# Kernel optimization log

Measured on AMD Instinct MI355X. Metric: run time of the kernel, lower is better.

## Reference

```python
import jax, jax.numpy as jnp
import numpy as np

NHEAD = 8
TOPKS = (8, 8)  # topk per level, coarse -> fine


def _to_bshd(x):
    # [B, C, H, W] -> [B, H*W, nhead, d]  (matches rearrange 'b c h w -> b (h w) c' + view)
    b, c, h, w = x.shape
    return jnp.transpose(x.reshape(b, c, h * w), (0, 2, 1)).reshape(b, h * w, NHEAD, c // NHEAD)


def _coarse_level(q, k, v, topk):
    b, c, h, w = k.shape
    d = c // NHEAD
    q_, k_, v_ = _to_bshd(q), _to_bshd(k), _to_bshd(v)
    temp = 1.0 / (d ** 0.5)
    A = jax.nn.softmax(jnp.einsum('nlhd,nshd->nlsh', q_, k_) * temp, axis=2)  # [b,L,S,h]
    _, idx = jax.lax.top_k(jnp.swapaxes(A, 2, 3), topk)  # [b,L,h,k]
    idx = jnp.swapaxes(idx, 2, 3)                        # [b,L,k,h]
    msg = jnp.einsum('nlsh,nshd->nlhd', A, v_)           # [b,L,h,d]
    topk_pos = jnp.stack([idx // w, idx % w])            # [2,b,L,k,h]
    return msg, topk_pos


def _fine_level(q, k, v, topk_pos, topk_prev, topk):
    b, c, h0, w0 = q.shape
    w1 = k.shape[3]
    d = c // NHEAD
    k_, v_ = _to_bshd(k), _to_bshd(v)
    H2, W2 = h0 // 2, w0 // 2
    L0 = H2 * W2
    # query grouped into 2x2 quads: [b, L0, 4, h, d]
    q_ = q.reshape(b, c, H2, 2, W2, 2).transpose(0, 2, 4, 3, 5, 1).reshape(b, L0, 4, NHEAD, d)
    tp = topk_pos * 2  # coarse positions -> fine grid
    cand = [(tp[0] + x) * w1 + tp[1] + y for x in (0, 1) for y in (0, 1)]
    t2 = topk_prev * 4
    idx = jnp.stack(cand, axis=3).reshape(b, L0, t2, NHEAD)  # [b,L,t2,h]
    idx_bh = idx.transpose(0, 3, 1, 2).reshape(b, NHEAD, L0 * t2)

    def gather(p):  # p: [b,S,h,d] -> gathered [b,L,t2,h,d]
        g = jnp.take_along_axis(jnp.swapaxes(p, 1, 2), idx_bh[..., None], axis=2)
        return g.reshape(b, NHEAD, L0, t2, d).transpose(0, 2, 3, 1, 4)

    tk, tv = gather(k_), gather(v_)
    temp = 1.0 / (d ** 0.5)
    A = jax.nn.softmax(jnp.einsum('blqhd,blthd->blqth', q_, tk) * temp, axis=3)  # [b,L,4,t2,h]
    _, ti = jax.lax.top_k(jnp.moveaxis(A, 3, 4), topk)  # [b,L,4,h,k]
    ti = jnp.moveaxis(ti, 4, 3)                         # [b,L,4,k,h]
    msg = jnp.einsum('blqth,blthd->blqhd', A, tv)       # [b,L,4,h,d]
    idx_b = jnp.broadcast_to(idx[:, :, None], (b, L0, 4, t2, NHEAD))
    gidx = jnp.take_along_axis(idx_b, ti, axis=3)       # [b,L,4,k,h] flat fine-grid indices
    gidx = gidx.reshape(b, H2, W2, 2, 2, topk, NHEAD).transpose(0, 1, 3, 2, 4, 5, 6)
    gidx = gidx.reshape(b, h0 * w0, topk, NHEAD)
    return msg, gidx


def _forward(q_fine, q_coarse, k_fine, k_coarse, v_fine, v_coarse, weight):
    msg0, topk_pos = _coarse_level(q_coarse, k_coarse, v_coarse, TOPKS[0])
    msg1, _ = _fine_level(q_fine, k_fine, v_fine, topk_pos, TOPKS[0], TOPKS[1])
    w = jax.nn.softmax(weight, axis=0)
    fm = msg0 * w[0]                  # [b,Lc,h,d]
    fm = fm[:, :, None] + msg1 * w[1]  # [b,Lc,4,h,d]
    b, Hc, Wc = q_coarse.shape[0], q_coarse.shape[2], q_coarse.shape[3]
    d = fm.shape[-1]
    # rearrange 'b (H W) (t1 t2) h d -> b (H t1 W t2) h d'
    fm = fm.reshape(b, Hc, Wc, 2, 2, NHEAD, d).transpose(0, 1, 3, 2, 4, 5, 6)
    return fm.reshape(b, Hc * Wc * 4, NHEAD, d)


def setup_inputs() -> dict:
    key = jax.random.key(0)
    ks = jax.random.split(key, 7)
    B, C = 4, 128
    return {
        'q_fine': jax.random.normal(ks[0], (B, C, 64, 64), jnp.float32),
        'q_coarse': jax.random.normal(ks[1], (B, C, 32, 32), jnp.float32),
        'k_fine': jax.random.normal(ks[2], (B, C, 64, 64), jnp.float32),
        'k_coarse': jax.random.normal(ks[3], (B, C, 32, 32), jnp.float32),
        'v_fine': jax.random.normal(ks[4], (B, C, 64, 64), jnp.float32),
        'v_coarse': jax.random.normal(ks[5], (B, C, 32, 32), jnp.float32),
        'weight': jax.random.normal(ks[6], (2,), jnp.float32),
    }


def reference(q_fine, q_coarse, k_fine, k_coarse, v_fine, v_coarse, weight):
    return _forward(q_fine, q_coarse, k_fine, k_coarse, v_fine, v_coarse, weight)
```

## Files before the change

kernel.cpp:

```cpp
#include <hip/hip_runtime.h>
#include <stdint.h>

#define TEMP 0.25f

typedef unsigned short u16;
typedef short v8s __attribute__((ext_vector_type(8)));
typedef float v4f __attribute__((ext_vector_type(4)));

static __device__ __forceinline__ uint32_t f2b_bits(float f){
    union { float f; uint32_t i; } x; x.f = f;
    uint32_t u = x.i;
    return (u + 0x7FFFu + ((u >> 16) & 1u)) >> 16;
}
static __device__ __forceinline__ float b2f(u16 u){
    union { uint32_t i; float f; } x; x.i = ((uint32_t)u) << 16; return x.f;
}
static __device__ __forceinline__ float bl(uint32_t u){
    union { uint32_t i; float f; } x; x.i = u << 16; return x.f;
}
static __device__ __forceinline__ float bh(uint32_t u){
    union { uint32_t i; float f; } x; x.i = u & 0xffff0000u; return x.f;
}
static __device__ __forceinline__ uint4 pack8(const uint32_t* e){
    return make_uint4(e[0] | (e[1] << 16), e[2] | (e[3] << 16),
                      e[4] | (e[5] << 16), e[6] | (e[7] << 16));
}
union U8S { uint4 u; v8s s; };
union I4S { int i[4]; v8s s; };
static __device__ __forceinline__ v8s asv8s(uint4 u){ U8S x; x.u = u; return x.s; }

template<int C>
static __device__ __forceinline__ float dppf(float x){
    int xi = __float_as_int(x);
    return __int_as_float(__builtin_amdgcn_update_dpp(xi, xi, C, 0xf, 0xf, false));
}
static __device__ __forceinline__ float red16_max(float m){
    m = fmaxf(m, dppf<0xB1>(m));  m = fmaxf(m, dppf<0x4E>(m));
    m = fmaxf(m, dppf<0x141>(m)); m = fmaxf(m, dppf<0x140>(m));
    return m;
}
static __device__ __forceinline__ float red16_sum(float s){
    s += dppf<0xB1>(s);  s += dppf<0x4E>(s);
    s += dppf<0x141>(s); s += dppf<0x140>(s);
    return s;
}
template<int C>
static __device__ __forceinline__ uint64_t dppmax64(uint64_t k){
    int hi = (int)(uint32_t)(k >> 32), lo = (int)(uint32_t)k;
    uint32_t oh = (uint32_t)__builtin_amdgcn_update_dpp(hi, hi, C, 0xf, 0xf, false);
    uint32_t ol = (uint32_t)__builtin_amdgcn_update_dpp(lo, lo, C, 0xf, 0xf, false);
    uint64_t ok = ((uint64_t)oh << 32) | ol;
    return ok > k ? ok : k;
}
static __device__ __forceinline__ uint64_t red16_maxkey(uint64_t k){
    k = dppmax64<0xB1>(k);  k = dppmax64<0x4E>(k);
    k = dppmax64<0x141>(k); k = dppmax64<0x140>(k);
    return k;
}

__global__ __launch_bounds__(256)
void pack_coarse(const float* __restrict__ kc, const float* __restrict__ vc,
                 uint4* __restrict__ KP1, uint4* __restrict__ KP3,
                 uint4* __restrict__ VP1)
{
    const int bh = blockIdx.x;
    const int kv = blockIdx.y;
    const int z  = blockIdx.z;
    const int b = bh >> 3, h = bh & 7;
    const int tid = threadIdx.x;
    const size_t sbase = (size_t)(b * 128 + h * 16) * 1024;
    const size_t fbase = (size_t)bh * 64 * 64;

    #pragma unroll
    for (int it = 0; it < 2; ++it){
        int task = it * 256 + tid;
        int kt = z * 8 + (task >> 6), ln = task & 63;
        int quad = ln >> 4, col = ln & 15;
        if (kv == 0){
            uint32_t e1[8], e3[8];
            #pragma unroll
            for (int j = 0; j < 8; ++j){
                int dch = (quad & 1) * 8 + j;
                float x = kc[sbase + (size_t)dch * 1024 + kt * 16 + col];
                uint32_t u0 = f2b_bits(x);
                float r1 = x - b2f((u16)u0);
                uint32_t u1 = f2b_bits(r1);
                float r2 = r1 - b2f((u16)u1);
                uint32_t u2 = f2b_bits(r2);
                e1[j] = (quad < 2) ? u0 : u1;
                e3[j] = (quad < 2) ? u2 : u0;
            }
            KP1[fbase + kt * 64 + ln] = pack8(e1);
            KP3[fbase + kt * 64 + ln] = pack8(e3);
        } else {
            uint32_t e[8];
            #pragma unroll
            for (int j = 0; j < 8; ++j){
                int key = kt * 16 + (quad & 1) * 8 + j;
                float x = vc[sbase + (size_t)col * 1024 + key];
                uint32_t u0 = f2b_bits(x);
                uint32_t u1 = f2b_bits(x - b2f((u16)u0));
                e[j] = (quad < 2) ? u0 : u1;
            }
            VP1[fbase + kt * 64 + ln] = pack8(e);
        }
    }
}

__global__ __launch_bounds__(256)
void pack_all(const float* __restrict__ kf, const float* __restrict__ vf,
              const float* __restrict__ qf,
              const float* __restrict__ kc, const float* __restrict__ vc,
              uint32_t* __restrict__ packed, float* __restrict__ qT,
              uint4* __restrict__ KP1, uint4* __restrict__ KP3,
              uint4* __restrict__ VP1)
{
    __shared__ float tile[64][129];
    const int bid = blockIdx.x;
    const int tid = threadIdx.x;

    if (bid < 768){
        const int pt = bid & 63, b = (bid >> 6) & 3, z = bid >> 8;
        const float* src = (z == 0) ? kf : (z == 1) ? vf : qf;
        const int pos0 = pt * 64;

        #pragma unroll
        for (int it = 0; it < 8; ++it){
            int task = it * 256 + tid;
            int ch = task >> 4, p4 = task & 15;
            float4 v = *(const float4*)(src + (size_t)(b * 128 + ch) * 4096 + pos0 + p4 * 4);
            tile[p4*4+0][ch] = v.x; tile[p4*4+1][ch] = v.y;
            tile[p4*4+2][ch] = v.z; tile[p4*4+3][ch] = v.w;
        }
        __syncthreads();

        if (z == 2){
            #pragma unroll
            for (int it = 0; it < 8; ++it){
                int task = it * 256 + tid;
                int p = task >> 5, c4 = task & 31;
                float4 v = make_float4(tile[p][c4*4+0], tile[p][c4*4+1],
                                       tile[p][c4*4+2], tile[p][c4*4+3]);
                *(float4*)(qT + ((size_t)(b * 4096) + pos0 + p) * 128 + c4 * 4) = v;
            }
        } else {
            const int x = pt;
            #pragma unroll
            for (int it = 0; it < 2; ++it){
                int task = it * 256 + tid;
                int hq = task >> 6, y = task & 63;
                int pprime = ((x >> 1) * 32 + (y >> 1)) * 4 + (x & 1) * 2 + (y & 1);
                size_t line = (size_t)(b * 8 + hq) * 4096 + pprime;
                uint32_t dw[8];
                #pragma unroll
                for (int i = 0; i < 8; ++i){
                    uint32_t lo = f2b_bits(tile[y][hq * 16 + 2 * i]);
                    uint32_t hi = f2b_bits(tile[y][hq * 16 + 2 * i + 1]);
                    dw[i] = lo | (hi << 16);
                }
                uint4* dst4 = (uint4*)packed + line * 4 + z * 2;
                dst4[0] = make_uint4(dw[0], dw[1], dw[2], dw[3]);
                dst4[1] = make_uint4(dw[4], dw[5], dw[6], dw[7]);
            }
        }
    } else {
        const int f2 = bid - 768;
        const int bh = f2 & 31, kv = (f2 >> 5) & 1, z = f2 >> 6;
        const int b = bh >> 3, h = bh & 7;
        const size_t sbase = (size_t)(b * 128 + h * 16) * 1024;
        const size_t fbase = (size_t)bh * 64 * 64;

        #pragma unroll
        for (int it = 0; it < 2; ++it){
            int task = it * 256 + tid;
            int kt = z * 8 + (task >> 6), ln = task & 63;
            int quad = ln >> 4, col = ln & 15;
            if (kv == 0){
                uint32_t e1[8], e3[8];
                #pragma unroll
                for (int j = 0; j < 8; ++j){
                    int dch = (quad & 1) * 8 + j;
                    float x = kc[sbase + (size_t)dch * 1024 + kt * 16 + col];
                    uint32_t u0 = f2b_bits(x);
                    float r1 = x - b2f((u16)u0);
                    uint32_t u1 = f2b_bits(r1);
                    float r2 = r1 - b2f((u16)u1);
                    uint32_t u2 = f2b_bits(r2);
                    e1[j] = (quad < 2) ? u0 : u1;
                    e3[j] = (quad < 2) ? u2 : u0;
                }
                KP1[fbase + kt * 64 + ln] = pack8(e1);
                KP3[fbase + kt * 64 + ln] = pack8(e3);
            } else {
                uint32_t e[8];
                #pragma unroll
                for (int j = 0; j < 8; ++j){
                    int key = kt * 16 + (quad & 1) * 8 + j;
                    float x = vc[sbase + (size_t)col * 1024 + key];
                    uint32_t xb = __float_as_uint(x);
                    uint32_t u0 = xb >> 16;
                    uint32_t u1 = f2b_bits(x - b2f((u16)u0));
                    e[j] = (quad < 2) ? u0 : u1;
                }
                VP1[fbase + kt * 64 + ln] = pack8(e);
            }
        }
    }
}

__global__ __launch_bounds__(256)
void coarse_mfma(const float* __restrict__ qc,
                 const uint4* __restrict__ KP1, const uint4* __restrict__ KP3,
                 const uint4* __restrict__ VP1,
                 float* __restrict__ msg0, int* __restrict__ topk_out)
{
    const int ltile = blockIdx.x;
    const int h = blockIdx.y, b = blockIdx.z;
    const int bh = b * 8 + h;
    const int tid = threadIdx.x, lane = tid & 63, wv = tid >> 6;
    const int quad = lane >> 4, col = lane & 15;
    const int lanex = lane ^ 32;
    const int lbase = ltile * 16;

    __shared__ uint32_t tls[4][16 * 20];
    __shared__ float rred[2][4][16];
    __shared__ float pvred[4][16][16];
    __shared__ float tkv[4][16][8];
    __shared__ int   tki[4][16][8];

    v8s a1, a3;
    {
        int row = lbase + col;
        int dch0 = (quad & 1) * 8;
        #pragma unroll
        for (int j = 0; j < 8; ++j){
            float x = qc[(size_t)(b * 128 + h * 16 + dch0 + j) * 1024 + row] * TEMP;
            uint32_t u0 = f2b_bits(x);
            float r1 = x - b2f((u16)u0);
            uint32_t u1 = f2b_bits(r1);
            float r2 = r1 - b2f((u16)u1);
            uint32_t u2 = f2b_bits(r2);
            a1[j] = (short)(quad < 2 ? u0 : u1);
            a3[j] = (short)(quad < 2 ? u0 : u2);
        }
    }

    const size_t fbase = (size_t)bh * 64 * 64;
    v4f sc[16];
    #pragma unroll
    for (int kt = 0; kt < 16; ++kt){
        int ktg = wv * 16 + kt;
        v8s b1 = asv8s(KP1[fbase + (size_t)ktg * 64 + lane]);
        v8s b2 = asv8s(KP1[fbase + (size_t)ktg * 64 + lanex]);
        v8s b3 = asv8s(KP3[fbase + (size_t)ktg * 64 + lane]);
        v4f c = {0.f, 0.f, 0.f, 0.f};
        c = __builtin_amdgcn_mfma_f32_16x16x32_bf16(a1, b1, c, 0, 0, 0);
        c = __builtin_amdgcn_mfma_f32_16x16x32_bf16(a1, b2, c, 0, 0, 0);
        c = __builtin_amdgcn_mfma_f32_16x16x32_bf16(a3, b3, c, 0, 0, 0);
        sc[kt] = c;
    }

    #pragma unroll
    for (int r = 0; r < 4; ++r){
        float m = sc[0][r];
        #pragma unroll
        for (int kt = 1; kt < 16; ++kt) m = fmaxf(m, sc[kt][r]);
        m = red16_max(m);
        if (col == 0) rred[0][wv][quad * 4 + r] = m;
    }
    __syncthreads();
    #pragma unroll
    for (int r = 0; r < 4; ++r){
        int row = quad * 4 + r;
        float m = fmaxf(fmaxf(rred[0][0][row], rred[0][1][row]),
                        fmaxf(rred[0][2][row], rred[0][3][row]));
        #pragma unroll
        for (int kt = 0; kt < 16; ++kt) sc[kt][r] = __expf(sc[kt][r] - m);
    }
    #pragma unroll
    for (int r = 0; r < 4; ++r){
        float s = 0.f;
        #pragma unroll
        for (int kt = 0; kt < 16; ++kt) s += sc[kt][r];
        s = red16_sum(s);
        if (col == 0) rred[1][wv][quad * 4 + r] = s;
    }

    v4f acc = {0.f, 0.f, 0.f, 0.f};
    uint32_t* tw = tls[wv];
    const int rdbase = col * 20 + 8 * (quad & 1);
    const uint32_t selp = (quad < 2) ? 0x05040100u : 0x07060302u;
    #pragma unroll
    for (int kt = 0; kt < 16; ++kt){
        #pragma unroll
        for (int r = 0; r < 4; ++r){
            float x = sc[kt][r];
            uint32_t u0 = __float_as_uint(x) >> 16;
            uint32_t u1 = f2b_bits(x - b2f((u16)u0));
            tw[(quad * 4 + r) * 20 + col] = u0 | (u1 << 16);
        }
        __builtin_amdgcn_s_waitcnt(0xC07F);
        uint4 d0 = *(const uint4*)&tw[rdbase];
        uint4 d1 = *(const uint4*)&tw[rdbase + 4];
        I4S ux;
        ux.i[0] = __builtin_amdgcn_perm(d0.y, d0.x, selp);
        ux.i[1] = __builtin_amdgcn_perm(d0.w, d0.z, selp);
        ux.i[2] = __builtin_amdgcn_perm(d1.y, d1.x, selp);
        ux.i[3] = __builtin_amdgcn_perm(d1.w, d1.z, selp);
        v8s ap = ux.s;
        v8s bv1 = asv8s(VP1[fbase + (size_t)(wv * 16 + kt) * 64 + lane]);
        v8s bv2 = asv8s(VP1[fbase + (size_t)(wv * 16 + kt) * 64 + lanex]);
        acc = __builtin_amdgcn_mfma_f32_16x16x32_bf16(ap, bv1, acc, 0, 0, 0);
        acc = __builtin_amdgcn_mfma_f32_16x16x32_bf16(ap, bv2, acc, 0, 0, 0);
    }
    #pragma unroll
    for (int r = 0; r < 4; ++r) pvred[wv][quad * 4 + r][col] = acc[r];

    #pragma unroll
    for (int r = 0; r < 4; ++r){
        int row = quad * 4 + r;
        #pragma unroll
        for (int rnd = 0; rnd < 8; ++rnd){
            float bv = sc[0][r]; int bk = 0;
            #pragma unroll
            for (int kt = 1; kt < 16; ++kt){
                bool g = sc[kt][r] > bv;
                bv = g ? sc[kt][r] : bv; bk = g ? kt : bk;
            }
            int bi = bk * 16 + col;
            uint64_t k = ((uint64_t)(uint32_t)__float_as_int(bv) << 32)
                       | (uint32_t)(~bi);
            k = red16_maxkey(k);
            bv = __int_as_float((int)(uint32_t)(k >> 32));
            bi = (int)(~(uint32_t)k);
            if ((bi & 15) == col){
                int ktw = bi >> 4;
                #pragma unroll
                for (int kt = 0; kt < 16; ++kt)
                    if (kt == ktw) sc[kt][r] = -1.0f;
            }
            if (col == rnd){ tkv[wv][row][rnd] = bv; tki[wv][row][rnd] = wv * 256 + bi; }
        }
    }
    __syncthreads();

    {
        int row = tid >> 4, dd = tid & 15;
        float v = pvred[0][row][dd] + pvred[1][row][dd] +
                  pvred[2][row][dd] + pvred[3][row][dd];
        float s = rred[1][0][row] + rred[1][1][row] +
                  rred[1][2][row] + rred[1][3][row];
        msg0[((size_t)((b * 1024 + lbase + row) * 8 + h)) * 16 + dd] = v / s;
    }
    if (tid < 16){
        int row = tid;
        int* tp = topk_out + (((b * 1024 + lbase + row) * 8 + h) * 8);
        int p[4] = {0, 0, 0, 0};
        #pragma unroll
        for (int rnd = 0; rnd < 8; ++rnd){
            float bv = -3.0f; int bw = 0, bi = 0x7fffffff;
            #pragma unroll
            for (int w = 0; w < 4; ++w){
                float v = tkv[w][row][p[w]];
                int   i = tki[w][row][p[w]];
                bool g = (v > bv) || (v == bv && i < bi);
                bv = g ? v : bv; bi = g ? i : bi; bw = g ? w : bw;
            }
            tp[rnd] = bi;
            p[bw]++;
        }
    }
}

__global__ __launch_bounds__(512, 2)
void coarse_kernel(const float* __restrict__ qc, const float* __restrict__ kc,
                   const float* __restrict__ vc, float* __restrict__ msg0,
                   int* __restrict__ topk_out)
{
    const int ltile = blockIdx.x;
    const int h = blockIdx.y, b = blockIdx.z;
    const int tid = threadIdx.x;
    const int lane = tid & 63, wv = tid >> 6;
    const int lbase = ltile * 32;
    __shared__ float sKV[16 * 1024];
    const size_t base = (size_t)(b * 128 + h * 16) * 1024;
    {
        const float4* gK = (const float4*)(kc + base);
        float4* lK = (float4*)sKV;
        #pragma unroll
        for (int i = 0; i < 8; ++i) lK[tid + 512 * i] = gK[tid + 512 * i];
    }
    float qreg[4];
    {
        int dq = lane & 15;
        #pragma unroll
        for (int li = 0; li < 4; ++li){
            int l = lbase + wv * 4 + li;
            qreg[li] = qc[base + (size_t)dq * 1024 + l] * TEMP;
        }
    }
    __syncthreads();
    float p[4][16];
    #pragma unroll
    for (int li = 0; li < 4; ++li)
        #pragma unroll
        for (int j = 0; j < 16; ++j) p[li][j] = 0.f;
    #pragma unroll
    for (int dch = 0; dch < 16; ++dch){
        float kf[16];
        #pragma unroll
        for (int ch = 0; ch < 4; ++ch){
            float4 kv = *(const float4*)&sKV[dch * 1024 + ch * 256 + (lane << 2)];
            kf[ch*4+0] = kv.x; kf[ch*4+1] = kv.y; kf[ch*4+2] = kv.z; kf[ch*4+3] = kv.w;
        }
        float qs[4];
        #pragma unroll
        for (int li = 0; li < 4; ++li) qs[li] = __shfl(qreg[li], dch);
        #pragma unroll
        for (int li = 0; li < 4; ++li)
            #pragma unroll
            for (int j = 0; j < 16; ++j) p[li][j] = fmaf(qs[li], kf[j], p[li][j]);
    }
    float invs[4];
    #pragma unroll
    for (int li = 0; li < 4; ++li){
        float m = p[li][0];
        #pragma unroll
        for (int j = 1; j < 16; ++j) m = fmaxf(m, p[li][j]);
        #pragma unroll
        for (int off = 32; off > 0; off >>= 1) m = fmaxf(m, __shfl_xor(m, off));
        float s = 0.f;
        #pragma unroll
        for (int j = 0; j < 16; ++j){ p[li][j] = __expf(p[li][j] - m); s += p[li][j]; }
        #pragma unroll
        for (int off = 32; off > 0; off >>= 1) s += __shfl_xor(s, off);
        invs[li] = 1.0f / s;
    }
    __syncthreads();
    {
        const float4* gV = (const float4*)(vc + base);
        float4* lV = (float4*)sKV;
        #pragma unroll
        for (int i = 0; i < 8; ++i) lV[tid + 512 * i] = gV[tid + 512 * i];
    }
    __syncthreads();
    float outv = 0.f;
    #pragma unroll
    for (int dd = 0; dd < 16; ++dd){
        float vf[16];
        #pragma unroll
        for (int ch = 0; ch < 4; ++ch){
            float4 vv = *(const float4*)&sKV[dd * 1024 + ch * 256 + (lane << 2)];
            vf[ch*4+0] = vv.x; vf[ch*4+1] = vv.y; vf[ch*4+2] = vv.z; vf[ch*4+3] = vv.w;
        }
        float a[4];
        #pragma unroll
        for (int li = 0; li < 4; ++li){
            float s = 0.f;
            #pragma unroll
            for (int j = 0; j < 16; ++j) s = fmaf(p[li][j], vf[j], s);
            a[li] = s;
        }
        #pragma unroll
        for (int off = 32; off > 0; off >>= 1)
            #pragma unroll
            for (int li = 0; li < 4; ++li) a[li] += __shfl_xor(a[li], off);
        #pragma unroll
        for (int li = 0; li < 4; ++li)
            outv = (lane == li * 16 + dd) ? a[li] * invs[li] : outv;
    }
    {
        int li = lane >> 4, dd = lane & 15;
        int l = lbase + wv * 4 + li;
        msg0[(size_t)((b * 1024 + l) * 8 + h) * 16 + dd] = outv;
    }
    const int lanebase = lane << 4;
    int mytk = 0;
    for (int r = 0; r < 8; ++r){
        float bv[4]; int bi[4];
        #pragma unroll
        for (int li = 0; li < 4; ++li){
            float v0[8]; int j0[8];
            #pragma unroll
            for (int k = 0; k < 8; ++k){
                bool g = p[li][2*k+1] > p[li][2*k];
                v0[k] = g ? p[li][2*k+1] : p[li][2*k];
                j0[k] = g ? 2*k+1 : 2*k;
            }
            float v1[4]; int j1[4];
            #pragma unroll
            for (int k = 0; k < 4; ++k){
                bool g = v0[2*k+1] > v0[2*k];
                v1[k] = g ? v0[2*k+1] : v0[2*k];
                j1[k] = g ? j0[2*k+1] : j0[2*k];
            }
            float v2[2]; int j2[2];
            #pragma unroll
            for (int k = 0; k < 2; ++k){
                bool g = v1[2*k+1] > v1[2*k];
                v2[k] = g ? v1[2*k+1] : v1[2*k];
                j2[k] = g ? j1[2*k+1] : j1[2*k];
            }
            bool g3 = v2[1] > v2[0];
            bv[li] = g3 ? v2[1] : v2[0];
            bi[li] = lanebase | (g3 ? j2[1] : j2[0]);
        }
        #pragma unroll
        for (int off = 32; off > 0; off >>= 1){
            #pragma unroll
            for (int li = 0; li < 4; ++li){
                float ov = __shfl_xor(bv[li], off);
                int   oi = __shfl_xor(bi[li], off);
                bool g = (ov > bv[li]) || (ov == bv[li] && oi < bi[li]);
                bv[li] = g ? ov : bv[li];
                bi[li] = g ? oi : bi[li];
            }
        }
        #pragma unroll
        for (int li = 0; li < 4; ++li){
            #pragma unroll
            for (int j = 0; j < 16; ++j)
                p[li][j] = (bi[li] == (lanebase | j)) ? -1.0f : p[li][j];
            mytk = (lane == li * 8 + r) ? bi[li] : mytk;
        }
    }
    if (lane < 32){
        int li = lane >> 3, r = lane & 7;
        int jw = mytk & 15, lw = mytk >> 4;
        int s = ((jw >> 2) << 8) | (lw << 2) | (jw & 3);
        int l = lbase + wv * 4 + li;
        topk_out[((b * 1024 + l) * 8 + h) * 8 + r] = s;
    }
}

__global__ __launch_bounds__(256)
void pack_kernel(const float* __restrict__ kf, const float* __restrict__ vf,
                 const float* __restrict__ qf,
                 uint32_t* __restrict__ packed, float* __restrict__ qT)
{
    const int pt = blockIdx.x;
    const int b  = blockIdx.y;
    const int z  = blockIdx.z;
    const float* src = (z == 0) ? kf : (z == 1) ? vf : qf;
    const int tid = threadIdx.x;
    __shared__ float tile[64][129];
    const int pos0 = pt * 64;

    #pragma unroll
    for (int it = 0; it < 8; ++it){
        int task = it * 256 + tid;
        int ch = task >> 4, p4 = task & 15;
        float4 v = *(const float4*)(src + (size_t)(b * 128 + ch) * 4096 + pos0 + p4 * 4);
        tile[p4*4+0][ch] = v.x; tile[p4*4+1][ch] = v.y;
        tile[p4*4+2][ch] = v.z; tile[p4*4+3][ch] = v.w;
    }
    __syncthreads();

    if (z == 2){
        #pragma unroll
        for (int it = 0; it < 8; ++it){
            int task = it * 256 + tid;
            int p = task >> 5, c4 = task & 31;
            float4 v = make_float4(tile[p][c4*4+0], tile[p][c4*4+1],
                                   tile[p][c4*4+2], tile[p][c4*4+3]);
            *(float4*)(qT + ((size_t)(b * 4096) + pos0 + p) * 128 + c4 * 4) = v;
        }
    } else {
        const int x = pt;
        #pragma unroll
        for (int it = 0; it < 2; ++it){
            int task = it * 256 + tid;
            int h = task >> 6, y = task & 63;
            int pprime = ((x >> 1) * 32 + (y >> 1)) * 4 + (x & 1) * 2 + (y & 1);
            size_t line = (size_t)(b * 8 + h) * 4096 + pprime;
            uint32_t dw[8];
            #pragma unroll
            for (int i = 0; i < 8; ++i){
                uint32_t lo = f2b_bits(tile[y][h * 16 + 2 * i]);
                uint32_t hi = f2b_bits(tile[y][h * 16 + 2 * i + 1]);
                dw[i] = lo | (hi << 16);
            }
            uint4* dst4 = (uint4*)packed + line * 4 + z * 2;
            dst4[0] = make_uint4(dw[0], dw[1], dw[2], dw[3]);
            dst4[1] = make_uint4(dw[4], dw[5], dw[6], dw[7]);
        }
    }
}

__global__ __launch_bounds__(256)
void fine_kernel(const float* __restrict__ qf, const float* __restrict__ kf,
                 const float* __restrict__ vf,
                 const float* __restrict__ qTg, const uint32_t* __restrict__ packed,
                 int transposed,
                 const float* __restrict__ wt,
                 const int* __restrict__ topk_in, const float* __restrict__ msg0,
                 float* __restrict__ out)
{
    const int l0 = blockIdx.x;
    const int b  = blockIdx.y;
    const int tid = threadIdx.x;

    __shared__ float vT[8][16][34];
    __shared__ float qT[8][4][16];
    __shared__ float pT[8][4][32];
    __shared__ int tkS[8][8];

    if (tid < 64) tkS[tid >> 3][tid & 7] =
        topk_in[((b * 1024 + l0) * 8 + (tid >> 3)) * 8 + (tid & 7)];
    __syncthreads();

    const int i = l0 >> 5, j = l0 & 31;
    const int hh = tid >> 5;
    const int t  = tid & 31;
    const int kk = t >> 2, cp = t & 3;

    float k[16];
    {
        int s = tkS[hh][kk];
        if (transposed){
            const uint4* pk = (const uint4*)packed;
            size_t line = (size_t)(b * 8 + hh) * 4096 + s * 4 + cp;
            uint4 a0 = pk[line*4+0], a1 = pk[line*4+1];
            uint4 a2 = pk[line*4+2], a3 = pk[line*4+3];
            k[0]=bl(a0.x);  k[1]=bh(a0.x);  k[2]=bl(a0.y);  k[3]=bh(a0.y);
            k[4]=bl(a0.z);  k[5]=bh(a0.z);  k[6]=bl(a0.w);  k[7]=bh(a0.w);
            k[8]=bl(a1.x);  k[9]=bh(a1.x);  k[10]=bl(a1.y); k[11]=bh(a1.y);
            k[12]=bl(a1.z); k[13]=bh(a1.z); k[14]=bl(a1.w); k[15]=bh(a1.w);
            vT[hh][0][t]=bl(a2.x);  vT[hh][1][t]=bh(a2.x);
            vT[hh][2][t]=bl(a2.y);  vT[hh][3][t]=bh(a2.y);
            vT[hh][4][t]=bl(a2.z);  vT[hh][5][t]=bh(a2.z);
            vT[hh][6][t]=bl(a2.w);  vT[hh][7][t]=bh(a2.w);
            vT[hh][8][t]=bl(a3.x);  vT[hh][9][t]=bh(a3.x);
            vT[hh][10][t]=bl(a3.y); vT[hh][11][t]=bh(a3.y);
            vT[hh][12][t]=bl(a3.z); vT[hh][13][t]=bh(a3.z);
            vT[hh][14][t]=bl(a3.w); vT[hh][15][t]=bh(a3.w);
        } else {
            int pos = (2 * (s >> 5) + (cp >> 1)) * 64 + 2 * (s & 31) + (cp & 1);
            size_t gb = (size_t)(b * 128 + hh * 16) * 4096 + pos;
            #pragma unroll
            for (int ch = 0; ch < 16; ++ch){
                k[ch] = kf[gb + (size_t)ch * 4096];
                vT[hh][ch][t] = vf[gb + (size_t)ch * 4096];
            }
        }
    }
    if (tid < 128){
        int qh = tid >> 4, aq = (tid >> 2) & 3, c4 = tid & 3;
        int qpos = (2 * i + (aq >> 1)) * 64 + 2 * j + (aq & 1);
        if (transposed){
            float4 u = *(const float4*)(qTg + ((size_t)(b * 4096) + qpos) * 128 + qh * 16 + c4 * 4);
            qT[qh][aq][c4*4+0] = u.x * TEMP;
            qT[qh][aq][c4*4+1] = u.y * TEMP;
            qT[qh][aq][c4*4+2] = u.z * TEMP;
            qT[qh][aq][c4*4+3] = u.w * TEMP;
        } else {
            #pragma unroll
            for (int c = 0; c < 4; ++c)
                qT[qh][aq][c4*4+c] =
                    qf[(size_t)(b * 128 + qh * 16 + c4 * 4 + c) * 4096 + qpos] * TEMP;
        }
    }
    __syncthreads();

    {
        float sc[4] = {0.f, 0.f, 0.f, 0.f};
        #pragma unroll
        for (int dch = 0; dch < 16; ++dch){
            float kv = k[dch];
            #pragma unroll
            for (int q = 0; q < 4; ++q) sc[q] = fmaf(qT[hh][q][dch], kv, sc[q]);
        }
        #pragma unroll
        for (int q = 0; q < 4; ++q){
            float m = sc[q];
            #pragma unroll
            for (int off = 16; off > 0; off >>= 1) m = fmaxf(m, __shfl_xor(m, off, 32));
            float e = __expf(sc[q] - m);
            float s = e;
            #pragma unroll
            for (int off = 16; off > 0; off >>= 1) s += __shfl_xor(s, off, 32);
            pT[hh][q][t] = e / s;
        }
    }
    __syncthreads();

    {
        float w0 = wt[0], w1 = wt[1];
        float mx = fmaxf(w0, w1);
        float e0 = __expf(w0 - mx), e1 = __expf(w1 - mx);
        float w0f = e0 / (e0 + e1), w1f = e1 / (e0 + e1);

        int q0 = (tid >> 4) & 1;
        int dd = tid & 15;
        float a0 = 0.f, a1 = 0.f;
        #pragma unroll
        for (int tt = 0; tt < 16; ++tt){
            float v0 = vT[hh][dd][tt * 2], v1 = vT[hh][dd][tt * 2 + 1];
            float2 pA = *(const float2*)&pT[hh][q0][tt * 2];
            float2 pB = *(const float2*)&pT[hh][q0 + 2][tt * 2];
            a0 = fmaf(pA.x, v0, a0); a0 = fmaf(pA.y, v1, a0);
            a1 = fmaf(pB.x, v0, a1); a1 = fmaf(pB.y, v1, a1);
        }
        float m0 = msg0[(size_t)((b * 1024 + l0) * 8 + hh) * 16 + dd];
        float o0 = w0f * m0 + w1f * a0;
        float o1 = w0f * m0 + w1f * a1;
        int posA = (2 * i) * 64 + 2 * j + q0;
        int posB = (2 * i + 1) * 64 + 2 * j + q0;
        out[(size_t)((b * 4096 + posA) * 8 + hh) * 16 + dd] = o0;
        out[(size_t)((b * 4096 + posB) * 8 + hh) * 16 + dd] = o1;
    }
}

extern "C" void kernel_launch(void* const* d_in, const int* in_sizes, int n_in,
                              void* d_out, int out_size, void* d_ws, size_t ws_size,
                              hipStream_t stream)
{
    (void)in_sizes; (void)n_in; (void)out_size;

    const float* q_fine   = (const float*)d_in[0];
    const float* q_coarse = (const float*)d_in[1];
    const float* k_fine   = (const float*)d_in[2];
    const float* k_coarse = (const float*)d_in[3];
    const float* v_fine   = (const float*)d_in[4];
    const float* v_coarse = (const float*)d_in[5];
    const float* weight   = (const float*)d_in[6];

    const size_t MB = 1024 * 1024;
    float*    msg0   = (float*)d_ws;
    int*      topk   = (int*)((char*)d_ws + 2 * MB);
    float*    qT     = (float*)((char*)d_ws + 3 * MB);
    uint32_t* packed = (uint32_t*)((char*)d_ws + 11 * MB);
    uint4*    KP1    = (uint4*)((char*)d_ws + 19 * MB);
    uint4*    KP3    = (uint4*)((char*)d_ws + 21 * MB);
    uint4*    VP1    = (uint4*)((char*)d_ws + 23 * MB);
    const int doT = (ws_size >= 19 * MB) ? 1 : 0;
    const int doM = (ws_size >= 25 * MB) ? 1 : 0;

    if (doM && doT){
        pack_all<<<dim3(1280), dim3(256), 0, stream>>>(k_fine, v_fine, q_fine,
                                                       k_coarse, v_coarse,
                                                       packed, qT, KP1, KP3, VP1);
        coarse_mfma<<<dim3(64, 8, 4), dim3(256), 0, stream>>>(q_coarse, KP1, KP3, VP1,
                                                              msg0, topk);
    } else {
        if (doM){
            pack_coarse<<<dim3(32, 2, 8), dim3(256), 0, stream>>>(k_coarse, v_coarse,
                                                                  KP1, KP3, VP1);
            coarse_mfma<<<dim3(64, 8, 4), dim3(256), 0, stream>>>(q_coarse, KP1, KP3, VP1,
                                                                  msg0, topk);
        } else {
            coarse_kernel<<<dim3(32, 8, 4), dim3(512), 0, stream>>>(q_coarse, k_coarse,
                                                                    v_coarse, msg0, topk);
        }
        if (doT){
            pack_kernel<<<dim3(64, 4, 3), dim3(256), 0, stream>>>(k_fine, v_fine, q_fine,
                                                                  packed, qT);
        }
    }

    fine_kernel<<<dim3(1024, 4), dim3(256), 0, stream>>>(q_fine, k_fine, v_fine,
                                                         qT, packed, doT,
                                                         weight, topk, msg0,
                                                         (float*)d_out);
}
```

Baseline: 196.4 us.

## Use packed bf16 split conversion, batch P tiles, DPP reductions, deferred topk stores

Replaces the manual hi/lo bf16 split with a single v_cvt_pk_bf16_f32 instruction in the V packing and in the probability staging. The P-to-LDS staging now writes two k-tiles per wait, so one waitcnt covers two MFMA pairs. The top-k winners are held in registers and written to shared memory once per row instead of once per round. In the fine-level softmax, the shuffle-based 32-lane reductions become DPP row reductions plus a ds_swizzle. It relies on inline asm for the gfx950 conversion instruction and doubles the tls shared buffer.

New measurement: 191.0 us. 1.03x faster.

```diff
diff --git a/kernel.cpp b/kernel.cpp
--- a/kernel.cpp
+++ b/kernel.cpp
@@ -25,6 +25,13 @@
     return make_uint4(e[0] | (e[1] << 16), e[2] | (e[3] << 16),
                       e[4] | (e[5] << 16), e[6] | (e[7] << 16));
 }
+static __device__ __forceinline__ uint32_t split2_pk(float x){
+    float hi = __uint_as_float(__float_as_uint(x) & 0xffff0000u);
+    float lo = x - hi;
+    uint32_t pk;
+    asm("v_cvt_pk_bf16_f32 %0, %1, %2" : "=v"(pk) : "v"(hi), "v"(lo));
+    return pk;
+}
 union U8S { uint4 u; v8s s; };
 union I4S { int i[4]; v8s s; };
 static __device__ __forceinline__ v8s asv8s(uint4 u){ U8S x; x.u = u; return x.s; }
@@ -43,6 +50,9 @@
     s += dppf<0xB1>(s);  s += dppf<0x4E>(s);
     s += dppf<0x141>(s); s += dppf<0x140>(s);
     return s;
+}
+static __device__ __forceinline__ float sw16(float x){
+    return __int_as_float(__builtin_amdgcn_ds_swizzle(__float_as_int(x), 0x401F));
 }
 template<int C>
 static __device__ __forceinline__ uint64_t dppmax64(uint64_t k){
@@ -197,10 +207,8 @@
                 for (int j = 0; j < 8; ++j){
                     int key = kt * 16 + (quad & 1) * 8 + j;
                     float x = vc[sbase + (size_t)col * 1024 + key];
-                    uint32_t xb = __float_as_uint(x);
-                    uint32_t u0 = xb >> 16;
-                    uint32_t u1 = f2b_bits(x - b2f((u16)u0));
-                    e[j] = (quad < 2) ? u0 : u1;
+                    uint32_t pk = split2_pk(x);
+                    e[j] = (quad < 2) ? (pk & 0xffffu) : (pk >> 16);
                 }
                 VP1[fbase + kt * 64 + ln] = pack8(e);
             }
@@ -222,7 +230,7 @@
     const int lanex = lane ^ 32;
     const int lbase = ltile * 16;
 
-    __shared__ uint32_t tls[4][16 * 20];
+    __shared__ uint32_t tls[4][2 * 320];
     __shared__ float rred[2][4][16];
     __shared__ float pvred[4][16][16];
     __shared__ float tkv[4][16][8];
@@ -291,27 +299,31 @@
     const int rdbase = col * 20 + 8 * (quad & 1);
     const uint32_t selp = (quad < 2) ? 0x05040100u : 0x07060302u;
     #pragma unroll
-    for (int kt = 0; kt < 16; ++kt){
-        #pragma unroll
-        for (int r = 0; r < 4; ++r){
-            float x = sc[kt][r];
-            uint32_t u0 = __float_as_uint(x) >> 16;
-            uint32_t u1 = f2b_bits(x - b2f((u16)u0));
-            tw[(quad * 4 + r) * 20 + col] = u0 | (u1 << 16);
+    for (int kb = 0; kb < 8; ++kb){
+        #pragma unroll
+        for (int ki = 0; ki < 2; ++ki){
+            int kt = kb * 2 + ki;
+            #pragma unroll
+            for (int r = 0; r < 4; ++r)
+                tw[ki * 320 + (quad * 4 + r) * 20 + col] = split2_pk(sc[kt][r]);
         }
         __builtin_amdgcn_s_waitcnt(0xC07F);
-        uint4 d0 = *(const uint4*)&tw[rdbase];
-        uint4 d1 = *(const uint4*)&tw[rdbase + 4];
-        I4S ux;
-        ux.i[0] = __builtin_amdgcn_perm(d0.y, d0.x, selp);
-        ux.i[1] = __builtin_amdgcn_perm(d0.w, d0.z, selp);
-        ux.i[2] = __builtin_amdgcn_perm(d1.y, d1.x, selp);
-        ux.i[3] = __builtin_amdgcn_perm(d1.w, d1.z, selp);
-        v8s ap = ux.s;
-        v8s bv1 = asv8s(VP1[fbase + (size_t)(wv * 16 + kt) * 64 + lane]);
-        v8s bv2 = asv8s(VP1[fbase + (size_t)(wv * 16 + kt) * 64 + lanex]);
-        acc = __builtin_amdgcn_mfma_f32_16x16x32_bf16(ap, bv1, acc, 0, 0, 0);
-        acc = __builtin_amdgcn_mfma_f32_16x16x32_bf16(ap, bv2, acc, 0, 0, 0);
+        #pragma unroll
+        for (int ki = 0; ki < 2; ++ki){
+            int kt = kb * 2 + ki;
+            uint4 d0 = *(const uint4*)&tw[ki * 320 + rdbase];
+            uint4 d1 = *(const uint4*)&tw[ki * 320 + rdbase + 4];
+            I4S ux;
+            ux.i[0] = __builtin_amdgcn_perm(d0.y, d0.x, selp);
+            ux.i[1] = __builtin_amdgcn_perm(d0.w, d0.z, selp);
+            ux.i[2] = __builtin_amdgcn_perm(d1.y, d1.x, selp);
+            ux.i[3] = __builtin_amdgcn_perm(d1.w, d1.z, selp);
+            v8s ap = ux.s;
+            v8s bv1 = asv8s(VP1[fbase + (size_t)(wv * 16 + kt) * 64 + lane]);
+            v8s bv2 = asv8s(VP1[fbase + (size_t)(wv * 16 + kt) * 64 + lanex]);
+            acc = __builtin_amdgcn_mfma_f32_16x16x32_bf16(ap, bv1, acc, 0, 0, 0);
+            acc = __builtin_amdgcn_mfma_f32_16x16x32_bf16(ap, bv2, acc, 0, 0, 0);
+        }
     }
     #pragma unroll
     for (int r = 0; r < 4; ++r) pvred[wv][quad * 4 + r][col] = acc[r];
@@ -319,6 +331,7 @@
     #pragma unroll
     for (int r = 0; r < 4; ++r){
         int row = quad * 4 + r;
+        float wval = 0.f; int widx = 0;
         #pragma unroll
         for (int rnd = 0; rnd < 8; ++rnd){
             float bv = sc[0][r]; int bk = 0;
@@ -339,8 +352,9 @@
                 for (int kt = 0; kt < 16; ++kt)
                     if (kt == ktw) sc[kt][r] = -1.0f;
             }
-            if (col == rnd){ tkv[wv][row][rnd] = bv; tki[wv][row][rnd] = wv * 256 + bi; }
-        }
+            if (col == rnd){ wval = bv; widx = wv * 256 + bi; }
+        }
+        if (col < 8){ tkv[wv][row][col] = wval; tki[wv][row][col] = widx; }
     }
     __syncthreads();
 
@@ -672,13 +686,11 @@
         }
         #pragma unroll
         for (int q = 0; q < 4; ++q){
-            float m = sc[q];
-            #pragma unroll
-            for (int off = 16; off > 0; off >>= 1) m = fmaxf(m, __shfl_xor(m, off, 32));
+            float m = red16_max(sc[q]);
+            m = fmaxf(m, sw16(m));
             float e = __expf(sc[q] - m);
-            float s = e;
-            #pragma unroll
-            for (int off = 16; off > 0; off >>= 1) s += __shfl_xor(s, off, 32);
+            float s = red16_sum(e);
+            s += sw16(s);
             pT[hh][q][t] = e / s;
         }
     }
```
